# Performance work log

Hardware: AMD Instinct MI355X
Metric: run time of the kernel (lower is better)

## Reference

```python
import jax, jax.numpy as jnp
import numpy as np

N, C, H, W, K = 8, 32, 512, 512, 6   # batch, embed dim, image HW, max components per image
MIN_PIX = 20
EPS = 1e-6
MARGIN = 0.5
L_INTER, L_INST, L_BG, L_SCENE = 0.4, 0.1, 0.2, 0.5


def _build_labels():
    # K disjoint 'subtitle line' rectangles per image; label 0 = background.
    # This is exactly what cv2.connectedComponents would return on the gt mask.
    labels = np.zeros((N, H, W), np.int32)
    for n in range(N):
        for k in range(K):
            r0 = 30 + k * 75
            c0 = 60 + (n % 3) * 20
            labels[n, r0:r0 + 40, c0:c0 + 300] = k + 1
    return labels


def setup_inputs() -> dict:
    key = jax.random.key(0)
    k1, k2 = jax.random.split(key)
    labels = _build_labels()
    gt = (labels > 0).astype(np.float32)[:, None]          # [N,1,H,W]
    color = jax.random.normal(k1, (N, C, H, W), jnp.float32)
    binary = jax.random.uniform(k2, (N, 1, H, W), jnp.float32)  # pred binary map
    return {"color": color, "gt": jnp.asarray(gt), "binary": binary,
            "comp_labels": jnp.asarray(labels)}


def _safe_norm(d2):
    # torch.norm = sqrt(sum sq); tiny floor avoids NaN grads at exactly 0
    return jnp.sqrt(jnp.maximum(d2, 1e-12))


def reference(color, gt, binary, comp_labels):
    f32 = color.dtype
    sub = (gt[:, 0] > 0.5).astype(f32)                                   # [N,H,W]
    text = (jax.lax.stop_gradient(binary)[:, 0] > 0.5).astype(f32)       # detached
    scene = text * (1.0 - sub)
    bg = (1.0 - sub) * (1.0 - scene)

    # one-hot component masks [N,K,H,W]
    comp = (comp_labels[:, None, :, :] ==
            jnp.arange(1, K + 1, dtype=comp_labels.dtype)[None, :, None, None]).astype(f32)
    cnt = comp.sum((2, 3))                                               # [N,K]

    # per-component first/second moments via batched segment-reduce
    S1 = jnp.einsum('nchw,nkhw->nkc', color, comp)                       # sum of feat
    fsq = (color * color).sum(1)                                         # [N,H,W]
    S2 = jnp.einsum('nhw,nkhw->nk', fsq, comp)                           # sum of |feat|^2
    m_inst = S1 / (cnt + EPS)[:, :, None]                                # [N,K,C]
    # sum over comp pixels of |f - m|^2, divided by (cnt+eps)
    intra_k = (S2 - 2.0 * (m_inst * S1).sum(-1)
               + cnt * (m_inst * m_inst).sum(-1)) / (cnt + EPS)

    sub_cnt = sub.sum((1, 2)); bg_cnt = bg.sum((1, 2)); scene_cnt = scene.sum((1, 2))
    m_sub = jnp.einsum('nchw,nhw->nc', color, sub) / (sub_cnt + EPS)[:, None]
    m_bg = jnp.einsum('nchw,nhw->nc', color, bg) / (bg_cnt + EPS)[:, None]
    m_scene = jnp.einsum('nchw,nhw->nc', color, scene) / (scene_cnt + EPS)[:, None]

    comp_big = cnt >= MIN_PIX                                            # [N,K]
    n_valid = comp_big.sum(1)                                            # [N]
    item_valid = (bg_cnt >= MIN_PIX) & (n_valid >= 1)
    cv = comp_big & item_valid[:, None]
    total = cv.sum()

    intra_sum = jnp.where(cv, intra_k, 0.0).sum()

    d_inst_bg = _safe_norm(((m_inst - m_bg[:, None, :]) ** 2).sum(-1))   # [N,K]
    inter_sum = jnp.where(cv, jax.nn.relu(MARGIN - d_inst_bg) ** 2, 0.0).sum()

    item_multi = item_valid & (n_valid > 1)
    d2_inst_sub = ((m_inst - m_sub[:, None, :]) ** 2).sum(-1)
    inst_sum = jnp.where(cv & item_multi[:, None], d2_inst_sub, 0.0).sum()
    inst_n = jnp.where(item_multi, n_valid, 0).sum()

    bg_cond = item_valid & (sub_cnt >= MIN_PIX)
    d_sub_bg = _safe_norm(((m_sub - m_bg) ** 2).sum(-1))
    subbg_sum = jnp.where(bg_cond, jax.nn.relu(MARGIN - d_sub_bg) ** 2, 0.0).sum()
    subbg_n = bg_cond.sum()

    sc_cond = item_valid & (scene_cnt >= MIN_PIX) & (sub_cnt >= MIN_PIX)
    d_sub_sc = _safe_norm(((m_sub - m_scene) ** 2).sum(-1))
    subsc_sum = jnp.where(sc_cond, jax.nn.relu(2.0 * MARGIN - d_sub_sc) ** 2, 0.0).sum()
    subsc_n = sc_cond.sum()

    def avg(s, n):
        return jnp.where(n > 0, s / jnp.maximum(n, 1).astype(f32), 0.0)

    loss = (avg(intra_sum, total)
            + L_INTER * avg(inter_sum, total)
            + L_INST * avg(inst_sum, inst_n)
            + L_BG * avg(subbg_sum, subbg_n)
            + L_SCENE * avg(subsc_sum, subsc_n))
    return jnp.where(total > 0, loss, jnp.zeros((), f32))
```

## Files before the change

### kernel.cpp

```cpp
#include <hip/hip_runtime.h>


#define NIMG   8
#define NCH    32
#define IMHW   (512 * 512)
#define STRIPE 2048
#define BPI    (IMHW / STRIPE)
#define WSN    304

__device__ __forceinline__ float redhalf(float x) {
    x += __shfl_xor(x, 1);
    x += __shfl_xor(x, 2);
    x += __shfl_xor(x, 4);
    x += __shfl_xor(x, 8);
    x += __shfl_xor(x, 16);
    return x;
}

__device__ __forceinline__ float red64(float x) {
    x += __shfl_xor(x, 1);
    x += __shfl_xor(x, 2);
    x += __shfl_xor(x, 4);
    x += __shfl_xor(x, 8);
    x += __shfl_xor(x, 16);
    x += __shfl_xor(x, 32);
    return x;
}

__global__ __launch_bounds__(256) void scl_main(
    const float* __restrict__ color, const float* __restrict__ gt,
    const float* __restrict__ bin, const int* __restrict__ lab,
    float* __restrict__ ws)
{
    __shared__ float lds[WSN];
    __shared__ unsigned int codes[STRIPE / 4];

    const int tid = threadIdx.x;
    for (int i = tid; i < WSN; i += 256) lds[i] = 0.f;

    const int n    = blockIdx.x / BPI;
    const int pix0 = (blockIdx.x % BPI) * STRIPE;

    const float* gtn  = gt  + (size_t)n * IMHW;
    const float* binn = bin + (size_t)n * IMHW;
    const int*   labn = lab + (size_t)n * IMHW;
    const float* coln = color + (size_t)n * NCH * IMHW;

    float cr0 = 0.f, cr1 = 0.f, cr2 = 0.f;
    float ck[6] = {0.f, 0.f, 0.f, 0.f, 0.f, 0.f};
#pragma unroll
    for (int j = 0; j < 2; ++j) {
        const int off = j * 1024 + (tid << 2);
        const int p   = pix0 + off;
        const float4 g4 = *reinterpret_cast<const float4*>(gtn + p);
        const float4 b4 = *reinterpret_cast<const float4*>(binn + p);
        const int4   l4 = *reinterpret_cast<const int4*>(labn + p);
        const float gg[4] = {g4.x, g4.y, g4.z, g4.w};
        const float bb[4] = {b4.x, b4.y, b4.z, b4.w};
        const int   ll[4] = {l4.x, l4.y, l4.z, l4.w};
        unsigned int wrd = 0;
#pragma unroll
        for (int e = 0; e < 4; ++e) {
            const bool sub  = gg[e] > 0.5f;
            const bool text = bb[e] > 0.5f;
            const int  r    = sub ? 0 : (text ? 1 : 2);
            const int  l    = ll[e];
            wrd |= (unsigned)((l << 2) | r) << (8 * e);
            cr0 += (r == 0) ? 1.f : 0.f;
            cr1 += (r == 1) ? 1.f : 0.f;
            cr2 += (r == 2) ? 1.f : 0.f;
#pragma unroll
            for (int kk = 0; kk < 6; ++kk)
                ck[kk] += (l == kk + 1) ? 1.f : 0.f;
        }
        codes[off >> 2] = wrd;
    }
    __syncthreads();

    cr0 = red64(cr0); cr1 = red64(cr1); cr2 = red64(cr2);
#pragma unroll
    for (int kk = 0; kk < 6; ++kk) ck[kk] = red64(ck[kk]);
    if ((tid & 63) == 0) {
        atomicAdd(&lds[288], cr0);
        atomicAdd(&lds[289], cr1);
        atomicAdd(&lds[290], cr2);
#pragma unroll
        for (int kk = 0; kk < 6; ++kk) atomicAdd(&lds[291 + kk], ck[kk]);
    }

    const int lane = tid & 63;
    const int wv   = tid >> 6;
    const int half = lane >> 5;
    const int l32  = lane & 31;

    for (int cpi = 0; cpi < 4; ++cpi) {
        const int cp = wv * 4 + cpi;
        const int c  = cp * 2 + half;
        const float* colc = coln + (size_t)c * IMHW;

        float r0 = 0.f, r1 = 0.f, r2 = 0.f;
        float ak[6]  = {0.f, 0.f, 0.f, 0.f, 0.f, 0.f};
        float as2[6] = {0.f, 0.f, 0.f, 0.f, 0.f, 0.f};

        for (int j = 0; j < STRIPE; j += 128) {
            const int off = j + (l32 << 2);
            const float4 v4 = *reinterpret_cast<const float4*>(colc + pix0 + off);
            const unsigned int cw = codes[off >> 2];
            const float vv[4] = {v4.x, v4.y, v4.z, v4.w};
#pragma unroll
            for (int e = 0; e < 4; ++e) {
                const float v = vv[e];
                const unsigned int cb = (cw >> (8 * e)) & 0xFFu;
                const int r = (int)(cb & 3u);
                const int l = (int)(cb >> 2);
                r0 += (r == 0) ? v : 0.f;
                r1 += (r == 1) ? v : 0.f;
                r2 += (r == 2) ? v : 0.f;
#pragma unroll
                for (int kk = 0; kk < 6; ++kk) {
                    const float mv = (l == kk + 1) ? v : 0.f;
                    ak[kk] += mv;
                    as2[kk] = fmaf(mv, mv, as2[kk]);
                }
            }
        }

        r0 = redhalf(r0); r1 = redhalf(r1); r2 = redhalf(r2);
#pragma unroll
        for (int kk = 0; kk < 6; ++kk) { ak[kk] = redhalf(ak[kk]); as2[kk] = redhalf(as2[kk]); }

        if (l32 == 0) {
            atomicAdd(&lds[ 0 + c], r0);
            atomicAdd(&lds[32 + c], r1);
            atomicAdd(&lds[64 + c], r2);
#pragma unroll
            for (int kk = 0; kk < 6; ++kk) {
                atomicAdd(&lds[96 + kk * 32 + c], ak[kk]);
                atomicAdd(&lds[297 + kk], as2[kk]);
            }
        }
    }
    __syncthreads();

    float* wsn = ws + (size_t)n * WSN;
    for (int i = tid; i < WSN; i += 256) {
        const float v = lds[i];
        if (v != 0.f) atomicAdd(&wsn[i], v);
    }
}

__global__ void scl_final(const float* __restrict__ ws, float* __restrict__ out)
{
    const int lane = threadIdx.x;
    const int n = lane / 6;
    const int k = lane - n * 6;
    const bool active = lane < 48;

    float t_cv = 0.f, t_intra = 0.f, t_inter = 0.f, t_inst = 0.f, t_instn = 0.f;
    float t_sbg = 0.f, t_sbgn = 0.f, t_ssc = 0.f, t_sscn = 0.f;

    if (active) {
        const float* w = ws + (size_t)n * WSN;
        const float cnt    = w[291 + k];
        const float s2     = w[297 + k];
        const float subc   = w[288];
        const float scenec = w[289];
        const float bgc    = w[290];

        float nv = 0.f;
#pragma unroll
        for (int kk = 0; kk < 6; ++kk) nv += (w[291 + kk] >= 20.f) ? 1.f : 0.f;

        const bool comp_big   = cnt >= 20.f;
        const bool item_valid = (bgc >= 20.f) && (nv >= 1.f);
        const bool cv         = comp_big && item_valid;

        const float den  = cnt + 1e-6f;
        const float dsub = subc + 1e-6f;
        const float dbg  = bgc + 1e-6f;
        const float dsc  = scenec + 1e-6f;

        float dot_mS1 = 0.f, dot_mm = 0.f, d2bg = 0.f, d2sub = 0.f;
        for (int c = 0; c < 32; ++c) {
            const float S1 = w[96 + k * 32 + c];
            const float m  = S1 / den;
            dot_mS1 = fmaf(m, S1, dot_mS1);
            dot_mm  = fmaf(m, m, dot_mm);
            const float msub = w[c] / dsub;
            const float mbg  = w[64 + c] / dbg;
            float d = m - mbg;  d2bg  = fmaf(d, d, d2bg);
            d = m - msub;       d2sub = fmaf(d, d, d2sub);
        }
        const float intra_k = (s2 - 2.f * dot_mS1 + cnt * dot_mm) / den;

        if (cv) {
            t_cv = 1.f;
            t_intra = intra_k;
            const float dd = sqrtf(fmaxf(d2bg, 1e-12f));
            const float r  = fmaxf(0.5f - dd, 0.f);
            t_inter = r * r;
        }
        const bool multi = item_valid && (nv > 1.f);
        if (cv && multi) t_inst = d2sub;

        if (k == 0) {
            if (multi) t_instn = nv;
            const bool bgcond = item_valid && (subc >= 20.f);
            const bool sccond = item_valid && (scenec >= 20.f) && (subc >= 20.f);
            float d2sb = 0.f, d2ss = 0.f;
            for (int c = 0; c < 32; ++c) {
                const float msub = w[c] / dsub;
                const float mbg  = w[64 + c] / dbg;
                const float msc  = w[32 + c] / dsc;
                float a = msub - mbg; d2sb = fmaf(a, a, d2sb);
                float b = msub - msc; d2ss = fmaf(b, b, d2ss);
            }
            if (bgcond) {
                const float dd = sqrtf(fmaxf(d2sb, 1e-12f));
                const float r  = fmaxf(0.5f - dd, 0.f);
                t_sbg = r * r; t_sbgn = 1.f;
            }
            if (sccond) {
                const float dd = sqrtf(fmaxf(d2ss, 1e-12f));
                const float r  = fmaxf(1.0f - dd, 0.f);
                t_ssc = r * r; t_sscn = 1.f;
            }
        }
    }

#define RED64(x) { x += __shfl_xor(x, 1); x += __shfl_xor(x, 2); x += __shfl_xor(x, 4); \
                   x += __shfl_xor(x, 8); x += __shfl_xor(x, 16); x += __shfl_xor(x, 32); }
    RED64(t_cv) RED64(t_intra) RED64(t_inter) RED64(t_inst) RED64(t_instn)
    RED64(t_sbg) RED64(t_sbgn) RED64(t_ssc) RED64(t_sscn)
#undef RED64

    if (lane == 0) {
        const float total = t_cv;
        auto avg = [](float s, float nn) { return nn > 0.f ? s / fmaxf(nn, 1.f) : 0.f; };
        const float loss = avg(t_intra, total)
                         + 0.4f * avg(t_inter, total)
                         + 0.1f * avg(t_inst, t_instn)
                         + 0.2f * avg(t_sbg, t_sbgn)
                         + 0.5f * avg(t_ssc, t_sscn);
        out[0] = (total > 0.f) ? loss : 0.f;
    }
}

extern "C" void kernel_launch(void* const* d_in, const int* in_sizes, int n_in,
                              void* d_out, int out_size, void* d_ws, size_t ws_size,
                              hipStream_t stream)
{
    (void)in_sizes; (void)n_in; (void)out_size; (void)ws_size;
    const float* color = (const float*)d_in[0];
    const float* gt    = (const float*)d_in[1];
    const float* bin   = (const float*)d_in[2];
    const int*   lab   = (const int*)d_in[3];
    float* ws  = (float*)d_ws;
    float* out = (float*)d_out;

    hipMemsetAsync(ws, 0, (size_t)NIMG * WSN * sizeof(float), stream);
    hipLaunchKernelGGL(scl_main, dim3(NIMG * BPI), dim3(256), 0, stream,
                       color, gt, bin, lab, ws);
    hipLaunchKernelGGL(scl_final, dim3(1), dim3(64), 0, stream, ws, out);
}
```

Measured before the change: 391.2 us.

## Specialize per-stripe accumulation to labels present, derive background from totals

Each block now records which component labels appear in its stripe and accumulates sums only for the first present label, running extra passes only when a stripe holds more than one. The per-pixel work drops from nine masked accumulators to five. Background sums and counts are no longer accumulated directly; they are reconstructed in the final kernel as the total minus the subtitle and scene sums. The stripe is halved to 1024 pixels and launch bounds request 8 blocks per CU for more parallelism, at the cost of more global atomics and some floating-point cancellation in the derived background mean.

```diff
diff --git a/kernel.cpp b/kernel.cpp
--- a/kernel.cpp
+++ b/kernel.cpp
@@ -4,7 +4,7 @@
 #define NIMG   8
 #define NCH    32
 #define IMHW   (512 * 512)
-#define STRIPE 2048
+#define STRIPE 1024
 #define BPI    (IMHW / STRIPE)
 #define WSN    304
 
@@ -27,16 +27,44 @@
     return x;
 }
 
-__global__ __launch_bounds__(256) void scl_main(
+__device__ __forceinline__ void comp_pass(
+    const float* __restrict__ colc, int pix0,
+    const unsigned* __restrict__ codes, int l32, int c, int L2, float* lds)
+{
+    float aL = 0.f, s2 = 0.f;
+#pragma unroll
+    for (int j = 0; j < STRIPE; j += 128) {
+        const int off = j + (l32 << 2);
+        const float4 v4 = *reinterpret_cast<const float4*>(colc + pix0 + off);
+        const unsigned cw = codes[off >> 2];
+        const float vv[4] = {v4.x, v4.y, v4.z, v4.w};
+#pragma unroll
+        for (int e = 0; e < 4; ++e) {
+            const int l = (int)((cw >> (8 * e + 2)) & 0x3Fu);
+            const float mv = (l == L2) ? vv[e] : 0.f;
+            aL += mv;
+            s2 = fmaf(mv, mv, s2);
+        }
+    }
+    aL = redhalf(aL); s2 = redhalf(s2);
+    if (l32 == 0 && L2 >= 1 && L2 <= 6) {
+        atomicAdd(&lds[96 + (L2 - 1) * 32 + c], aL);
+        atomicAdd(&lds[297 + (L2 - 1)], s2);
+    }
+}
+
+__global__ __launch_bounds__(256, 8) void scl_main(
     const float* __restrict__ color, const float* __restrict__ gt,
     const float* __restrict__ bin, const int* __restrict__ lab,
     float* __restrict__ ws)
 {
     __shared__ float lds[WSN];
-    __shared__ unsigned int codes[STRIPE / 4];
+    __shared__ unsigned codes[STRIPE / 4];
+    __shared__ int labmask;
 
     const int tid = threadIdx.x;
     for (int i = tid; i < WSN; i += 256) lds[i] = 0.f;
+    if (tid == 0) labmask = 0;
 
     const int n    = blockIdx.x / BPI;
     const int pix0 = (blockIdx.x % BPI) * STRIPE;
@@ -46,19 +74,18 @@
     const int*   labn = lab + (size_t)n * IMHW;
     const float* coln = color + (size_t)n * NCH * IMHW;
 
-    float cr0 = 0.f, cr1 = 0.f, cr2 = 0.f;
-    float ck[6] = {0.f, 0.f, 0.f, 0.f, 0.f, 0.f};
-#pragma unroll
-    for (int j = 0; j < 2; ++j) {
-        const int off = j * 1024 + (tid << 2);
-        const int p   = pix0 + off;
+    const int off1 = tid << 2;
+    {
+        const int p = pix0 + off1;
         const float4 g4 = *reinterpret_cast<const float4*>(gtn + p);
         const float4 b4 = *reinterpret_cast<const float4*>(binn + p);
         const int4   l4 = *reinterpret_cast<const int4*>(labn + p);
         const float gg[4] = {g4.x, g4.y, g4.z, g4.w};
         const float bb[4] = {b4.x, b4.y, b4.z, b4.w};
         const int   ll[4] = {l4.x, l4.y, l4.z, l4.w};
-        unsigned int wrd = 0;
+        unsigned wrd = 0; int lm = 0;
+        float c0 = 0.f, c1 = 0.f;
+        float ck[6] = {0.f, 0.f, 0.f, 0.f, 0.f, 0.f};
 #pragma unroll
         for (int e = 0; e < 4; ++e) {
             const bool sub  = gg[e] > 0.5f;
@@ -66,27 +93,34 @@
             const int  r    = sub ? 0 : (text ? 1 : 2);
             const int  l    = ll[e];
             wrd |= (unsigned)((l << 2) | r) << (8 * e);
-            cr0 += (r == 0) ? 1.f : 0.f;
-            cr1 += (r == 1) ? 1.f : 0.f;
-            cr2 += (r == 2) ? 1.f : 0.f;
+            lm  |= 1 << l;
+            c0  += (r == 0) ? 1.f : 0.f;
+            c1  += (r == 1) ? 1.f : 0.f;
 #pragma unroll
             for (int kk = 0; kk < 6; ++kk)
                 ck[kk] += (l == kk + 1) ? 1.f : 0.f;
         }
-        codes[off >> 2] = wrd;
+        codes[tid] = wrd;
+        __syncthreads();
+
+        c0 = red64(c0); c1 = red64(c1);
+#pragma unroll
+        for (int kk = 0; kk < 6; ++kk) ck[kk] = red64(ck[kk]);
+        lm |= __shfl_xor(lm, 1);  lm |= __shfl_xor(lm, 2);
+        lm |= __shfl_xor(lm, 4);  lm |= __shfl_xor(lm, 8);
+        lm |= __shfl_xor(lm, 16); lm |= __shfl_xor(lm, 32);
+        if ((tid & 63) == 0) {
+            atomicAdd(&lds[288], c0);
+            atomicAdd(&lds[289], c1);
+#pragma unroll
+            for (int kk = 0; kk < 6; ++kk) atomicAdd(&lds[291 + kk], ck[kk]);
+            atomicOr(&labmask, lm);
+        }
     }
     __syncthreads();
 
-    cr0 = red64(cr0); cr1 = red64(cr1); cr2 = red64(cr2);
-#pragma unroll
-    for (int kk = 0; kk < 6; ++kk) ck[kk] = red64(ck[kk]);
-    if ((tid & 63) == 0) {
-        atomicAdd(&lds[288], cr0);
-        atomicAdd(&lds[289], cr1);
-        atomicAdd(&lds[290], cr2);
-#pragma unroll
-        for (int kk = 0; kk < 6; ++kk) atomicAdd(&lds[291 + kk], ck[kk]);
-    }
+    const unsigned cmask = ((unsigned)labmask) & ~1u;
+    const int Lc = cmask ? (__ffs(cmask) - 1) : 255;
 
     const int lane = tid & 63;
     const int wv   = tid >> 6;
@@ -98,46 +132,48 @@
         const int c  = cp * 2 + half;
         const float* colc = coln + (size_t)c * IMHW;
 
-        float r0 = 0.f, r1 = 0.f, r2 = 0.f;
-        float ak[6]  = {0.f, 0.f, 0.f, 0.f, 0.f, 0.f};
-        float as2[6] = {0.f, 0.f, 0.f, 0.f, 0.f, 0.f};
-
+        float vt = 0.f, s0 = 0.f, s1 = 0.f, aL = 0.f, s2 = 0.f;
+#pragma unroll
         for (int j = 0; j < STRIPE; j += 128) {
             const int off = j + (l32 << 2);
             const float4 v4 = *reinterpret_cast<const float4*>(colc + pix0 + off);
-            const unsigned int cw = codes[off >> 2];
+            const unsigned cw = codes[off >> 2];
             const float vv[4] = {v4.x, v4.y, v4.z, v4.w};
 #pragma unroll
             for (int e = 0; e < 4; ++e) {
                 const float v = vv[e];
-                const unsigned int cb = (cw >> (8 * e)) & 0xFFu;
-                const int r = (int)(cb & 3u);
-                const int l = (int)(cb >> 2);
-                r0 += (r == 0) ? v : 0.f;
-                r1 += (r == 1) ? v : 0.f;
-                r2 += (r == 2) ? v : 0.f;
-#pragma unroll
-                for (int kk = 0; kk < 6; ++kk) {
-                    const float mv = (l == kk + 1) ? v : 0.f;
-                    ak[kk] += mv;
-                    as2[kk] = fmaf(mv, mv, as2[kk]);
-                }
-            }
-        }
-
-        r0 = redhalf(r0); r1 = redhalf(r1); r2 = redhalf(r2);
-#pragma unroll
-        for (int kk = 0; kk < 6; ++kk) { ak[kk] = redhalf(ak[kk]); as2[kk] = redhalf(as2[kk]); }
+                const int r = (int)((cw >> (8 * e)) & 3u);
+                const int l = (int)((cw >> (8 * e + 2)) & 0x3Fu);
+                vt += v;
+                s0 += (r == 0) ? v : 0.f;
+                s1 += (r == 1) ? v : 0.f;
+                const float mv = (l == Lc) ? v : 0.f;
+                aL += mv;
+                s2 = fmaf(mv, mv, s2);
+            }
+        }
+
+        vt = redhalf(vt); s0 = redhalf(s0); s1 = redhalf(s1);
+        aL = redhalf(aL); s2 = redhalf(s2);
 
         if (l32 == 0) {
-            atomicAdd(&lds[ 0 + c], r0);
-            atomicAdd(&lds[32 + c], r1);
-            atomicAdd(&lds[64 + c], r2);
-#pragma unroll
-            for (int kk = 0; kk < 6; ++kk) {
-                atomicAdd(&lds[96 + kk * 32 + c], ak[kk]);
-                atomicAdd(&lds[297 + kk], as2[kk]);
-            }
+            atomicAdd(&lds[ 0 + c], s0);
+            atomicAdd(&lds[32 + c], s1);
+            atomicAdd(&lds[64 + c], vt);
+            if (Lc <= 6) {
+                atomicAdd(&lds[96 + (Lc - 1) * 32 + c], aL);
+                atomicAdd(&lds[297 + (Lc - 1)], s2);
+            }
+        }
+    }
+
+    unsigned extra = cmask ? (cmask & (cmask - 1)) : 0u;
+    while (extra) {
+        const int L2 = __ffs(extra) - 1; extra &= extra - 1;
+        for (int cpi = 0; cpi < 4; ++cpi) {
+            const int cp = wv * 4 + cpi;
+            const int c  = cp * 2 + half;
+            comp_pass(coln + (size_t)c * IMHW, pix0, codes, l32, c, L2, lds);
         }
     }
     __syncthreads();
@@ -165,7 +201,7 @@
         const float s2     = w[297 + k];
         const float subc   = w[288];
         const float scenec = w[289];
-        const float bgc    = w[290];
+        const float bgc    = 262144.f - subc - scenec;
 
         float nv = 0.f;
 #pragma unroll
@@ -187,7 +223,7 @@
             dot_mS1 = fmaf(m, S1, dot_mS1);
             dot_mm  = fmaf(m, m, dot_mm);
             const float msub = w[c] / dsub;
-            const float mbg  = w[64 + c] / dbg;
+            const float mbg  = (w[64 + c] - w[c] - w[32 + c]) / dbg;
             float d = m - mbg;  d2bg  = fmaf(d, d, d2bg);
             d = m - msub;       d2sub = fmaf(d, d, d2sub);
         }
@@ -210,7 +246,7 @@
             float d2sb = 0.f, d2ss = 0.f;
             for (int c = 0; c < 32; ++c) {
                 const float msub = w[c] / dsub;
-                const float mbg  = w[64 + c] / dbg;
+                const float mbg  = (w[64 + c] - w[c] - w[32 + c]) / dbg;
                 const float msc  = w[32 + c] / dsc;
                 float a = msub - mbg; d2sb = fmaf(a, a, d2sb);
                 float b = msub - msc; d2ss = fmaf(b, b, d2ss);
```

Result: slower. 404.8 us (+3.5%).
